# Kernel optimization log

Hardware: AMD Instinct MI355X
Metric: run time of the kernel (lower is better)

## Reference

```python
import jax, jax.numpy as jnp
import numpy as np

DIM = 1024
N_HEADS = 16
HEAD_DIM = DIM // N_HEADS
B, T = 2, 2048


def setup_inputs() -> dict:
    key = jax.random.key(0)
    ks = jax.random.split(key, 5)
    s = 0.02
    return {
        "x": jax.random.normal(ks[0], (B, T, DIM), dtype=jnp.float32),
        "w_qkv": jax.random.normal(ks[1], (DIM, 3 * DIM), dtype=jnp.float32) * s,
        "b_qkv": jnp.zeros((3 * DIM,), dtype=jnp.float32),
        "w_proj": jax.random.normal(ks[2], (DIM, DIM), dtype=jnp.float32) * s,
        "b_proj": jnp.zeros((DIM,), dtype=jnp.float32),
    }


def reference(x, w_qkv, b_qkv, w_proj, b_proj):
    Bb, Tt, C = x.shape
    H, Dh = N_HEADS, HEAD_DIM
    qkv = x @ w_qkv + b_qkv                       # [B,T,3C]
    qkv = qkv.reshape(Bb, Tt, 3, H, Dh)
    q = jnp.transpose(qkv[:, :, 0], (0, 2, 1, 3))  # [B,H,T,Dh]
    k = jnp.transpose(qkv[:, :, 1], (0, 2, 1, 3))
    v = jnp.transpose(qkv[:, :, 2], (0, 2, 1, 3))
    att = jnp.einsum("bhqd,bhkd->bhqk", q, k) / jnp.sqrt(jnp.float32(Dh))
    causal = jnp.tril(jnp.ones((Tt, Tt), dtype=bool))
    att = jnp.where(causal[None, None], att, -jnp.inf)
    att = jax.nn.softmax(att, axis=-1)
    out = jnp.einsum("bhqk,bhkd->bhqd", att, v)    # [B,H,T,Dh]
    out = jnp.transpose(out, (0, 2, 1, 3)).reshape(Bb, Tt, C)
    return out @ w_proj + b_proj
```

## Files before the change

kernel.cpp:

```cpp
#include <hip/hip_runtime.h>
#include <math.h>

#define DIMC 1024
#define NH 16
#define HD 64
#define BATCH 2
#define SEQ 2048
#define M_ROWS (BATCH * SEQ)
#define QKV_N (3 * DIMC)

typedef __attribute__((ext_vector_type(8))) short bf16x8;
typedef __attribute__((ext_vector_type(4))) float f32x4;
typedef __attribute__((ext_vector_type(2))) unsigned int u32x2;

static __device__ __forceinline__ unsigned short f2bf(float f) {
    union { float f; unsigned u; } v; v.f = f;
    unsigned r = v.u + 0x7fffu + ((v.u >> 16) & 1u);
    return (unsigned short)(r >> 16);
}

static __device__ __forceinline__ unsigned cvt_pk_bf16(float lo, float hi) {
    unsigned r;
    asm("v_cvt_pk_bf16_f32 %0, %1, %2" : "=v"(r) : "v"(lo), "v"(hi));
    return r;
}

#define GLOAD16(g, l)                                                          \
    __builtin_amdgcn_global_load_lds(                                          \
        (__attribute__((address_space(1))) void*)(void*)(g),                   \
        (__attribute__((address_space(3))) void*)(void*)(l), 16, 0, 0)

__global__ __launch_bounds__(256) void cvt_bf16(const float* __restrict__ in,
                                                short* __restrict__ out)
{
    int i = blockIdx.x * 256 + threadIdx.x;
    float4 v = reinterpret_cast<const float4*>(in)[i];
    ushort4 o = {f2bf(v.x), f2bf(v.y), f2bf(v.z), f2bf(v.w)};
    reinterpret_cast<ushort4*>(out)[i] = o;
}

__global__ __launch_bounds__(256) void transpose_bf16(const float* __restrict__ in,
                                                      short* __restrict__ out,
                                                      int R, int C)
{
    __shared__ short tile[64][65];
    const int tid = threadIdx.x;
    const int r0 = blockIdx.y * 64, c0 = blockIdx.x * 64;
    #pragma unroll
    for (int i = 0; i < 4; ++i) {
        int r = i * 16 + (tid >> 4);
        int c = (tid & 15) * 4;
        float4 v = *reinterpret_cast<const float4*>(&in[(size_t)(r0 + r) * C + c0 + c]);
        tile[c + 0][r] = f2bf(v.x);
        tile[c + 1][r] = f2bf(v.y);
        tile[c + 2][r] = f2bf(v.z);
        tile[c + 3][r] = f2bf(v.w);
    }
    __syncthreads();
    #pragma unroll
    for (int i = 0; i < 4; ++i) {
        int c = i * 16 + (tid >> 4);
        int r = (tid & 15) * 4;
        ushort4 o;
        o.x = tile[c][r + 0]; o.y = tile[c][r + 1];
        o.z = tile[c][r + 2]; o.w = tile[c][r + 3];
        *reinterpret_cast<ushort4*>(&out[(size_t)(c0 + c) * R + r0 + r]) = o;
    }
}

template<int EPI>
__global__ __launch_bounds__(256) void gemm_mfma(const short* __restrict__ A,
                                                 const short* __restrict__ Bt,
                                                 const float* __restrict__ bias,
                                                 float* __restrict__ C,
                                                 short* __restrict__ Qb,
                                                 short* __restrict__ Kb,
                                                 short* __restrict__ Vt,
                                                 int M, int N, int K)
{
    __shared__ short As[128 * 32];
    __shared__ short Bs[128 * 32];

    const int tid  = threadIdx.x;
    const int wave = tid >> 6;
    const int lane = tid & 63;
    const int l16  = lane & 15;
    const int lg   = lane >> 4;
    const int wr   = wave >> 1;
    const int wc   = wave & 1;

    const int brow = blockIdx.y * 128;
    const int bcol = blockIdx.x * 128;

    const int srow   = tid >> 2;
    const int schunk = (tid & 3) * 8;
    const short* ga0 = A  + (size_t)(brow + srow) * K + schunk;
    const short* gb0 = Bt + (size_t)(bcol + srow) * K + schunk;

    f32x4 acc[4][4] = {};

    for (int k0 = 0; k0 < K; k0 += 32) {
        __syncthreads();
        GLOAD16(ga0 + k0,          &As[tid * 8]);
        GLOAD16(ga0 + 64 * K + k0, &As[2048 + tid * 8]);
        GLOAD16(gb0 + k0,          &Bs[tid * 8]);
        GLOAD16(gb0 + 64 * K + k0, &Bs[2048 + tid * 8]);
        __syncthreads();

        bf16x8 af[4], bf[4];
        #pragma unroll
        for (int m = 0; m < 4; ++m)
            af[m] = *reinterpret_cast<const bf16x8*>(
                &As[(wr * 64 + m * 16 + l16) * 32 + lg * 8]);
        #pragma unroll
        for (int n = 0; n < 4; ++n)
            bf[n] = *reinterpret_cast<const bf16x8*>(
                &Bs[(wc * 64 + n * 16 + l16) * 32 + lg * 8]);
        #pragma unroll
        for (int m = 0; m < 4; ++m)
            #pragma unroll
            for (int n = 0; n < 4; ++n)
                acc[m][n] = __builtin_amdgcn_mfma_f32_16x16x32_bf16(
                    af[m], bf[n], acc[m][n], 0, 0, 0);
    }

    if (EPI == 0) {
        #pragma unroll
        for (int m = 0; m < 4; ++m) {
            #pragma unroll
            for (int n = 0; n < 4; ++n) {
                int col = bcol + wc * 64 + n * 16 + l16;
                float bv = bias[col];
                #pragma unroll
                for (int r = 0; r < 4; ++r) {
                    int row = brow + wr * 64 + m * 16 + lg * 4 + r;
                    C[(size_t)row * N + col] = acc[m][n][r] + bv;
                }
            }
        }
    } else {
        const int sec = bcol >> 10;
        #pragma unroll
        for (int m = 0; m < 4; ++m) {
            const int t0 = brow + wr * 64 + m * 16 + lg * 4;
            const int bb = t0 >> 11;
            const int tl = t0 & 2047;
            #pragma unroll
            for (int n = 0; n < 4; ++n) {
                int col = bcol + wc * 64 + n * 16 + l16;
                int hh  = (col & 1023) >> 6;
                int d   = col & 63;
                float bv = bias[col];
                if (sec == 0) {
                    #pragma unroll
                    for (int r = 0; r < 4; ++r)
                        Qb[((size_t)(bb * NH + hh) * SEQ + tl + r) * HD + d] =
                            (short)f2bf((acc[m][n][r] + bv) * 0.18033688011112042f);
                } else if (sec == 1) {
                    #pragma unroll
                    for (int r = 0; r < 4; ++r)
                        Kb[((size_t)(bb * NH + hh) * SEQ + tl + r) * HD + d] =
                            (short)f2bf(acc[m][n][r] + bv);
                } else {
                    ushort4 o;
                    o.x = f2bf(acc[m][n][0] + bv);
                    o.y = f2bf(acc[m][n][1] + bv);
                    o.z = f2bf(acc[m][n][2] + bv);
                    o.w = f2bf(acc[m][n][3] + bv);
                    *reinterpret_cast<ushort4*>(
                        &Vt[((size_t)(bb * NH + hh) * HD + d) * SEQ + tl]) = o;
                }
            }
        }
    }
}

__global__ __launch_bounds__(256, 2) void attn_mfma(const short* __restrict__ Qb,
                                                    const short* __restrict__ Kb,
                                                    const short* __restrict__ Vt,
                                                    short* __restrict__ out)
{
    const int tid  = threadIdx.x;
    const int wave = tid >> 6;
    const int lane = tid & 63;
    const int l16  = lane & 15;
    const int lg   = lane >> 4;

    const int raw = blockIdx.x;
    const int wg  = (raw & 7) * 64 + (raw >> 3);
    const int i = wg & 15;
    const int h = (wg >> 4) & 15;
    const int b = wg >> 8;

    const int wp  = wave >> 1;
    const int wro = (wave & 1) * 16;
    const int qtA = 2 * i + wp;
    const int qtB = 63 - 2 * i - wp;
    const int ktA = i;
    const int ktB = 31 - i;

    __shared__ short ksh[64 * 64];
    __shared__ short vsh[64 * 64];
    __shared__ short pshB[4][16 * 64];
    __shared__ short pshA[4][16 * 64];

    const short* qgb = Qb + (size_t)(b * NH + h) * SEQ * HD;
    bf16x8 qfA[2], qfB[2];
    {
        const short* qa = qgb + (size_t)(qtA * 32 + wro + l16) * HD;
        qfA[0] = *reinterpret_cast<const bf16x8*>(qa + 8 * lg);
        qfA[1] = *reinterpret_cast<const bf16x8*>(qa + 32 + 8 * lg);
        const short* qb = qgb + (size_t)(qtB * 32 + wro + l16) * HD;
        qfB[0] = *reinterpret_cast<const bf16x8*>(qb + 8 * lg);
        qfB[1] = *reinterpret_cast<const bf16x8*>(qb + 32 + 8 * lg);
    }

    const short* kgb = Kb + (size_t)(b * NH + h) * SEQ * HD;
    const short* vgb = Vt + (size_t)(b * NH + h) * HD * SEQ;

    const int row0 = tid >> 3;
    const int col0 = (tid & 7) * 8;

    bf16x8 kreg[2], vreg[2];
    #pragma unroll
    for (int it = 0; it < 2; ++it) {
        int row = row0 + it * 32;
        kreg[it] = *reinterpret_cast<const bf16x8*>(kgb + (size_t)row * HD + col0);
        vreg[it] = *reinterpret_cast<const bf16x8*>(vgb + (size_t)row * SEQ + col0);
    }

    f32x4 accA[4] = {}, accB[4] = {};
    float lsumA = 0.f, lsumB = 0.f;

    const int qlocA = (qtA & 1) * 32 + wro + l16;
    const int qlocB = (qtB & 1) * 32 + wro + l16;
    char* pwB = (char*)pshB[wave];
    char* pwA = (char*)pshA[wave];
    const char* kshc = (const char*)ksh;
    const char* vshc = (const char*)vsh;
    const f32x4 fzero = {0.f, 0.f, 0.f, 0.f};

    for (int kt = 0; kt <= ktB; ++kt) {
        __syncthreads();
        #pragma unroll
        for (int it = 0; it < 2; ++it) {
            int row  = row0 + it * 32;
            int byte = (row << 7) + (col0 << 1);
            byte ^= ((row & 7) << 4);
            *reinterpret_cast<bf16x8*>((char*)ksh + byte) = kreg[it];
            *reinterpret_cast<bf16x8*>((char*)vsh + byte) = vreg[it];
        }
        if (kt < ktB) {
            #pragma unroll
            for (int it = 0; it < 2; ++it) {
                int row = row0 + it * 32;
                kreg[it] = *reinterpret_cast<const bf16x8*>(
                    kgb + (size_t)((kt + 1) * 64 + row) * HD + col0);
                vreg[it] = *reinterpret_cast<const bf16x8*>(
                    vgb + (size_t)row * SEQ + (kt + 1) * 64 + col0);
            }
        }
        __syncthreads();

        const bool doA = (kt <= ktA);

        f32x4 saB[4], saA[4];
        __builtin_amdgcn_s_setprio(1);
        #pragma unroll
        for (int kc = 0; kc < 4; ++kc) {
            saB[kc] = fzero;
            int row = kc * 16 + l16;
            #pragma unroll
            for (int c = 0; c < 2; ++c) {
                int byte = (row << 7) + (c << 6) + (lg << 4);
                byte ^= ((row & 7) << 4);
                bf16x8 kf = *reinterpret_cast<const bf16x8*>(kshc + byte);
                saB[kc] = __builtin_amdgcn_mfma_f32_16x16x32_bf16(kf, qfB[c], saB[kc], 0, 0, 0);
            }
        }
        if (doA) {
            #pragma unroll
            for (int kc = 0; kc < 4; ++kc) {
                saA[kc] = fzero;
                int row = kc * 16 + l16;
                #pragma unroll
                for (int c = 0; c < 2; ++c) {
                    int byte = (row << 7) + (c << 6) + (lg << 4);
                    byte ^= ((row & 7) << 4);
                    bf16x8 kf = *reinterpret_cast<const bf16x8*>(kshc + byte);
                    saA[kc] = __builtin_amdgcn_mfma_f32_16x16x32_bf16(kf, qfA[c], saA[kc], 0, 0, 0);
                }
            }
        }
        __builtin_amdgcn_s_setprio(0);

        {
            const bool mB = (kt == ktB);
            #pragma unroll
            for (int kc = 0; kc < 4; ++kc) {
                const int kl = kc * 16 + lg * 4;
                float s0 = saB[kc][0], s1 = saB[kc][1], s2 = saB[kc][2], s3 = saB[kc][3];
                if (mB) {
                    if (kl + 0 > qlocB) s0 = -1e30f;
                    if (kl + 1 > qlocB) s1 = -1e30f;
                    if (kl + 2 > qlocB) s2 = -1e30f;
                    if (kl + 3 > qlocB) s3 = -1e30f;
                }
                float p0 = exp2f(s0), p1 = exp2f(s1), p2 = exp2f(s2), p3 = exp2f(s3);
                lsumB += (p0 + p1) + (p2 + p3);
                u32x2 pk;
                pk.x = cvt_pk_bf16(p0, p1);
                pk.y = cvt_pk_bf16(p2, p3);
                int byte = (l16 << 7) + (kc << 5) + (lg << 3);
                byte ^= ((l16 & 7) << 4);
                *reinterpret_cast<u32x2*>(pwB + byte) = pk;
            }
        }
        if (doA) {
            const bool mA = (kt == ktA);
            #pragma unroll
            for (int kc = 0; kc < 4; ++kc) {
                const int kl = kc * 16 + lg * 4;
                float s0 = saA[kc][0], s1 = saA[kc][1], s2 = saA[kc][2], s3 = saA[kc][3];
                if (mA) {
                    if (kl + 0 > qlocA) s0 = -1e30f;
                    if (kl + 1 > qlocA) s1 = -1e30f;
                    if (kl + 2 > qlocA) s2 = -1e30f;
                    if (kl + 3 > qlocA) s3 = -1e30f;
                }
                float p0 = exp2f(s0), p1 = exp2f(s1), p2 = exp2f(s2), p3 = exp2f(s3);
                lsumA += (p0 + p1) + (p2 + p3);
                u32x2 pk;
                pk.x = cvt_pk_bf16(p0, p1);
                pk.y = cvt_pk_bf16(p2, p3);
                int byte = (l16 << 7) + (kc << 5) + (lg << 3);
                byte ^= ((l16 & 7) << 4);
                *reinterpret_cast<u32x2*>(pwA + byte) = pk;
            }
        }

        __builtin_amdgcn_s_setprio(1);
        #pragma unroll
        for (int c = 0; c < 2; ++c) {
            int pbyte = (l16 << 7) + (c << 6) + (lg << 4);
            pbyte ^= ((l16 & 7) << 4);
            bf16x8 pfB = *reinterpret_cast<const bf16x8*>(pwB + pbyte);
            #pragma unroll
            for (int dg = 0; dg < 4; ++dg) {
                int vrow  = dg * 16 + l16;
                int vbyte = (vrow << 7) + (c << 6) + (lg << 4);
                vbyte ^= ((vrow & 7) << 4);
                bf16x8 vf = *reinterpret_cast<const bf16x8*>(vshc + vbyte);
                accB[dg] = __builtin_amdgcn_mfma_f32_16x16x32_bf16(pfB, vf, accB[dg], 0, 0, 0);
            }
        }
        if (doA) {
            #pragma unroll
            for (int c = 0; c < 2; ++c) {
                int pbyte = (l16 << 7) + (c << 6) + (lg << 4);
                pbyte ^= ((l16 & 7) << 4);
                bf16x8 pfA = *reinterpret_cast<const bf16x8*>(pwA + pbyte);
                #pragma unroll
                for (int dg = 0; dg < 4; ++dg) {
                    int vrow  = dg * 16 + l16;
                    int vbyte = (vrow << 7) + (c << 6) + (lg << 4);
                    vbyte ^= ((vrow & 7) << 4);
                    bf16x8 vf = *reinterpret_cast<const bf16x8*>(vshc + vbyte);
                    accA[dg] = __builtin_amdgcn_mfma_f32_16x16x32_bf16(pfA, vf, accA[dg], 0, 0, 0);
                }
            }
        }
        __builtin_amdgcn_s_setprio(0);
    }

    lsumA += __shfl_xor(lsumA, 16);
    lsumA += __shfl_xor(lsumA, 32);
    lsumB += __shfl_xor(lsumB, 16);
    lsumB += __shfl_xor(lsumB, 32);
    const float linvA = 1.0f / lsumA;
    const float linvB = 1.0f / lsumB;

    #pragma unroll
    for (int r = 0; r < 4; ++r) {
        float invA = __shfl(linvA, lg * 4 + r);
        float invB = __shfl(linvB, lg * 4 + r);
        int qa = qtA * 32 + wro + lg * 4 + r;
        int qb = qtB * 32 + wro + lg * 4 + r;
        short* opa = out + ((size_t)(b * SEQ + qa)) * DIMC + h * HD;
        short* opb = out + ((size_t)(b * SEQ + qb)) * DIMC + h * HD;
        #pragma unroll
        for (int dg = 0; dg < 4; ++dg) {
            opa[dg * 16 + l16] = (short)f2bf(accA[dg][r] * invA);
            opb[dg * 16 + l16] = (short)f2bf(accB[dg][r] * invB);
        }
    }
}

extern "C" void kernel_launch(void* const* d_in, const int* in_sizes, int n_in,
                              void* d_out, int out_size, void* d_ws, size_t ws_size,
                              hipStream_t stream)
{
    const float* x      = (const float*)d_in[0];
    const float* w_qkv  = (const float*)d_in[1];
    const float* b_qkv  = (const float*)d_in[2];
    const float* w_proj = (const float*)d_in[3];
    const float* b_proj = (const float*)d_in[4];
    float* out = (float*)d_out;

    short* Qb   = (short*)d_ws;
    short* Kb   = Qb + (size_t)M_ROWS * DIMC;
    short* Vt   = Kb + (size_t)M_ROWS * DIMC;
    short* attn = Vt + (size_t)M_ROWS * DIMC;
    short* xb   = attn + (size_t)M_ROWS * DIMC;
    short* Wqt  = xb + (size_t)M_ROWS * DIMC;
    short* Wpt  = Wqt + (size_t)DIMC * QKV_N;

    cvt_bf16<<<dim3(M_ROWS * DIMC / 4 / 256), dim3(256), 0, stream>>>(x, xb);
    transpose_bf16<<<dim3(QKV_N / 64, DIMC / 64), dim3(256), 0, stream>>>(
        w_qkv, Wqt, DIMC, QKV_N);
    transpose_bf16<<<dim3(DIMC / 64, DIMC / 64), dim3(256), 0, stream>>>(
        w_proj, Wpt, DIMC, DIMC);

    gemm_mfma<1><<<dim3(QKV_N / 128, M_ROWS / 128), dim3(256), 0, stream>>>(
        xb, Wqt, b_qkv, nullptr, Qb, Kb, Vt, M_ROWS, QKV_N, DIMC);

    attn_mfma<<<dim3(BATCH * NH * 16), dim3(256), 0, stream>>>(Qb, Kb, Vt, attn);

    gemm_mfma<0><<<dim3(DIMC / 128, M_ROWS / 128), dim3(256), 0, stream>>>(
        attn, Wpt, b_proj, out, nullptr, nullptr, nullptr, M_ROWS, DIMC, DIMC);
}
```

Baseline: 122.5 us.

## Double the GEMM K-tile to 64 and remap workgroups across XCDs

The bf16 MFMA GEMM now loads a 64-wide K slab per iteration into two 32-wide LDS sub-tiles. This halves the number of barrier-separated load/compute rounds. Workgroup indices are also permuted so that consecutive workgroups, which are dispatched round-robin across the eight XCDs, land on contiguous output tiles to improve L2 locality. The remap hardcodes 32 row-blocks (M=4096) and assumes the workgroup count divides by 8. LDS use doubles, which may reduce occupancy.

```diff
diff --git a/kernel.cpp b/kernel.cpp
--- a/kernel.cpp
+++ b/kernel.cpp
@@ -78,8 +78,8 @@
                                                  short* __restrict__ Vt,
                                                  int M, int N, int K)
 {
-    __shared__ short As[128 * 32];
-    __shared__ short Bs[128 * 32];
+    __shared__ short As[2][128 * 32];
+    __shared__ short Bs[2][128 * 32];
 
     const int tid  = threadIdx.x;
     const int wave = tid >> 6;
@@ -89,39 +89,54 @@
     const int wr   = wave >> 1;
     const int wc   = wave & 1;
 
-    const int brow = blockIdx.y * 128;
-    const int bcol = blockIdx.x * 128;
-
-    const int srow   = tid >> 2;
-    const int schunk = (tid & 3) * 8;
-    const short* ga0 = A  + (size_t)(brow + srow) * K + schunk;
-    const short* gb0 = Bt + (size_t)(bcol + srow) * K + schunk;
+    const int nx   = gridDim.x;
+    const int flat = blockIdx.y * nx + blockIdx.x;
+    const int nwg  = nx * gridDim.y;
+    const int q8   = nwg >> 3;
+    const int nf   = (flat & 7) * q8 + (flat >> 3);
+    const int by   = nf & 31;
+    const int bx   = nf >> 5;
+
+    const int brow = by * 128;
+    const int bcol = bx * 128;
+
+    const short* ga = A  + (size_t)brow * K;
+    const short* gb = Bt + (size_t)bcol * K;
 
     f32x4 acc[4][4] = {};
 
-    for (int k0 = 0; k0 < K; k0 += 32) {
+    for (int k0 = 0; k0 < K; k0 += 64) {
         __syncthreads();
-        GLOAD16(ga0 + k0,          &As[tid * 8]);
-        GLOAD16(ga0 + 64 * K + k0, &As[2048 + tid * 8]);
-        GLOAD16(gb0 + k0,          &Bs[tid * 8]);
-        GLOAD16(gb0 + 64 * K + k0, &Bs[2048 + tid * 8]);
+        #pragma unroll
+        for (int li = 0; li < 4; ++li) {
+            int c   = li * 256 + tid;
+            int ks  = c >> 9;
+            int row = (c & 511) >> 2;
+            int sub = c & 3;
+            size_t goff = (size_t)row * K + k0 + ks * 32 + sub * 8;
+            GLOAD16(ga + goff, &As[0][0] + c * 8);
+            GLOAD16(gb + goff, &Bs[0][0] + c * 8);
+        }
         __syncthreads();
 
-        bf16x8 af[4], bf[4];
-        #pragma unroll
-        for (int m = 0; m < 4; ++m)
-            af[m] = *reinterpret_cast<const bf16x8*>(
-                &As[(wr * 64 + m * 16 + l16) * 32 + lg * 8]);
-        #pragma unroll
-        for (int n = 0; n < 4; ++n)
-            bf[n] = *reinterpret_cast<const bf16x8*>(
-                &Bs[(wc * 64 + n * 16 + l16) * 32 + lg * 8]);
-        #pragma unroll
-        for (int m = 0; m < 4; ++m)
+        #pragma unroll
+        for (int ks = 0; ks < 2; ++ks) {
+            bf16x8 af[4], bf[4];
+            #pragma unroll
+            for (int m = 0; m < 4; ++m)
+                af[m] = *reinterpret_cast<const bf16x8*>(
+                    &As[ks][(wr * 64 + m * 16 + l16) * 32 + lg * 8]);
             #pragma unroll
             for (int n = 0; n < 4; ++n)
-                acc[m][n] = __builtin_amdgcn_mfma_f32_16x16x32_bf16(
-                    af[m], bf[n], acc[m][n], 0, 0, 0);
+                bf[n] = *reinterpret_cast<const bf16x8*>(
+                    &Bs[ks][(wc * 64 + n * 16 + l16) * 32 + lg * 8]);
+            #pragma unroll
+            for (int m = 0; m < 4; ++m)
+                #pragma unroll
+                for (int n = 0; n < 4; ++n)
+                    acc[m][n] = __builtin_amdgcn_mfma_f32_16x16x32_bf16(
+                        af[m], bf[n], acc[m][n], 0, 0, 0);
+        }
     }
 
     if (EPI == 0) {
```

After: 116.0 us. -5.3%, faster.
